# Performance work log

Measured on AMD Instinct MI355X. Metric: run time of the kernel, lower is better.

Reference implementation:

```python
import jax, jax.numpy as jnp
import numpy as np

OBS_DIM = 115
ID_LO, ID_HI = 97, 108  # one-hot agent-id slice


def setup_inputs() -> dict:
    key = jax.random.key(0)
    k1, k2 = jax.random.split(key)
    a, b, n_agents = 128, 512, 11
    state_dim = n_agents * OBS_DIM  # 1265
    agents_q = jax.random.normal(k1, (a, b, n_agents), dtype=jnp.float32)
    global_state = jax.random.normal(k2, (a, b, state_dim), dtype=jnp.float32)
    return {"agents_q": agents_q, "global_state": global_state}


def reference(agents_q, global_state):
    a, b, n_agents = agents_q.shape
    q = agents_q.reshape(-1, n_agents)                 # [B, A]
    gs = global_state.reshape(-1, global_state.shape[-1])  # [B, A*115]
    B = q.shape[0]

    ball_pos = gs[:, 88:90]                            # [B, 2]
    holder_info = gs[:, 94:97]
    is_my_team = holder_info[:, 1] != 0                # .bool() semantics
    goal = jnp.array([1.0, 0.0], dtype=q.dtype)
    ball_goal_dist = jnp.sqrt(jnp.sum((ball_pos - goal) ** 2, axis=1))
    valid_advance = is_my_team & (ball_goal_dist > 0.19) & (ball_goal_dist < 0.99)

    # all agent obs blocks at once: [B, A, 115]
    obs = gs[:, : n_agents * OBS_DIM].reshape(B, n_agents, OBS_DIM)
    agent_id = jnp.argmax(obs[:, :, ID_LO:ID_HI], axis=-1)        # [B, A] in [0,10]
    pos_x = jnp.take_along_axis(obs, (2 * agent_id)[..., None], axis=-1)[..., 0]
    pos_y = jnp.take_along_axis(obs, (2 * agent_id + 1)[..., None], axis=-1)[..., 0]

    # distance of each agent to ball and to goal: [B, A]
    dist_matrix = jnp.sqrt((pos_x - ball_pos[:, 0:1]) ** 2 + (pos_y - ball_pos[:, 1:2]) ** 2)
    goal_dist_matrix = jnp.sqrt((pos_x - 1.0) ** 2 + pos_y ** 2)

    holder_mask = jax.nn.one_hot(jnp.argmin(dist_matrix, axis=1), n_agents, dtype=q.dtype)
    advance_component = holder_mask * valid_advance[:, None].astype(q.dtype) * 5.0
    position_component = 1.0 / (goal_dist_matrix + 1e-6)
    combined = jnp.where(valid_advance[:, None], advance_component, position_component)

    weights = jax.nn.softmax(combined, axis=1)
    global_q = jnp.sum(q * weights, axis=1, keepdims=True)        # [B, 1]
    return (global_q * n_agents).reshape(a, b, 1)
```

## Files before the change

### kernel.cpp

```cpp
#include <hip/hip_runtime.h>
#include <math.h>

#define OBS_DIM 115
#define N_AGENTS 11

__global__ __launch_bounds__(256) void qmix_kernel(
    const float* __restrict__ q,
    const float* __restrict__ gs,
    float* __restrict__ out,
    int B)
{
    int r = blockIdx.x * blockDim.x + threadIdx.x;
    if (r >= B) return;

    const float* row = gs + (long)r * (N_AGENTS * OBS_DIM);

    float bx = row[88];
    float by = row[89];
    float team = row[95];
    float gx0 = bx - 1.0f;
    float ball_goal_dist = sqrtf(gx0 * gx0 + by * by);
    bool valid = (team != 0.0f) && (ball_goal_dist > 0.19f) && (ball_goal_dist < 0.99f);

    float dist[N_AGENTS];
    float gd[N_AGENTS];

    #pragma unroll
    for (int a = 0; a < N_AGENTS; ++a) {
        const float* base = row + a * OBS_DIM;
        float best = base[97];
        int bi = 0;
        #pragma unroll
        for (int j = 1; j < 11; ++j) {
            float v = base[97 + j];
            if (v > best) { best = v; bi = j; }
        }
        float px = base[2 * bi];
        float py = base[2 * bi + 1];
        float ddx = px - bx;
        float ddy = py - by;
        dist[a] = sqrtf(ddx * ddx + ddy * ddy);
        float ggx = px - 1.0f;
        gd[a] = sqrtf(ggx * ggx + py * py);
    }

    int holder = 0;
    float dmin = dist[0];
    #pragma unroll
    for (int a = 1; a < N_AGENTS; ++a) {
        if (dist[a] < dmin) { dmin = dist[a]; holder = a; }
    }

    float comb[N_AGENTS];
    float m = -INFINITY;
    #pragma unroll
    for (int a = 0; a < N_AGENTS; ++a) {
        float c;
        if (valid) {
            c = (a == holder) ? 5.0f : 0.0f;
        } else {
            c = 1.0f / (gd[a] + 1e-6f);
        }
        comb[a] = c;
        m = fmaxf(m, c);
    }

    const float* qr = q + (long)r * N_AGENTS;
    float s = 0.0f;
    float acc = 0.0f;
    #pragma unroll
    for (int a = 0; a < N_AGENTS; ++a) {
        float w = expf(comb[a] - m);
        s += w;
        acc += qr[a] * w;
    }

    out[r] = acc * (float)N_AGENTS / s;
}

extern "C" void kernel_launch(void* const* d_in, const int* in_sizes, int n_in,
                              void* d_out, int out_size, void* d_ws, size_t ws_size,
                              hipStream_t stream) {
    const float* q  = (const float*)d_in[0];
    const float* gs = (const float*)d_in[1];
    float* out = (float*)d_out;

    int B = in_sizes[0] / N_AGENTS;
    const int block = 256;
    int grid = (B + block - 1) / block;
    qmix_kernel<<<grid, block, 0, stream>>>(q, gs, out, B);
}
```

Measured before the change: 404.6 us.

## Stage needed row columns into shared memory via coalesced wave loads

Each block now handles 32 rows. Each wave cooperatively gathers only the columns needed (the position and one-hot slices, the ball and team fields, and q) into shared memory with lane-contiguous accesses, and then one thread per row computes the result from shared memory. This replaces per-thread strided, uncoalesced global loads. In exchange it uses about 49KB of LDS per block, which limits occupancy, and only 32 threads do the compute.

Result: slower. 419.0 us (+3.6%).

```diff
diff --git a/kernel.cpp b/kernel.cpp
--- a/kernel.cpp
+++ b/kernel.cpp
@@ -3,6 +3,9 @@
 
 #define OBS_DIM 115
 #define N_AGENTS 11
+#define ROWS 32
+#define SROW 385
+#define TELEM 377
 
 __global__ __launch_bounds__(256) void qmix_kernel(
     const float* __restrict__ q,
@@ -10,72 +13,112 @@
     float* __restrict__ out,
     int B)
 {
-    int r = blockIdx.x * blockDim.x + threadIdx.x;
-    if (r >= B) return;
+    __shared__ float sm[ROWS * SROW];
 
-    const float* row = gs + (long)r * (N_AGENTS * OBS_DIM);
+    const int tid  = threadIdx.x;
+    const int wave = tid >> 6;
+    const int lane = tid & 63;
+    const int row0 = blockIdx.x * ROWS;
 
-    float bx = row[88];
-    float by = row[89];
-    float team = row[95];
-    float gx0 = bx - 1.0f;
-    float ball_goal_dist = sqrtf(gx0 * gx0 + by * by);
-    bool valid = (team != 0.0f) && (ball_goal_dist > 0.19f) && (ball_goal_dist < 0.99f);
-
-    float dist[N_AGENTS];
-    float gd[N_AGENTS];
+    int cols[6];
+    #pragma unroll
+    for (int it = 0; it < 6; ++it) {
+        int o = it * 64 + lane;
+        int col;
+        if (o < 363) {
+            int a = o / 33;
+            int j = o - a * 33;
+            col = a * OBS_DIM + (j < 22 ? j : j + 75);
+        } else if (o == 363) col = 88;
+        else if (o == 364) col = 89;
+        else                col = 95;
+        cols[it] = col;
+    }
 
     #pragma unroll
-    for (int a = 0; a < N_AGENTS; ++a) {
-        const float* base = row + a * OBS_DIM;
-        float best = base[97];
-        int bi = 0;
+    for (int rr = 0; rr < 8; ++rr) {
+        int r = wave * 8 + rr;
+        int rg = row0 + r;
+        if (rg < B) {
+            long gbase = (long)rg * (N_AGENTS * OBS_DIM);
+            long qbase = (long)rg * N_AGENTS;
+            #pragma unroll
+            for (int it = 0; it < 6; ++it) {
+                int o = it * 64 + lane;
+                if (o < 366) {
+                    sm[r * SROW + o] = gs[gbase + cols[it]];
+                } else if (o < TELEM) {
+                    sm[r * SROW + o] = q[qbase + (o - 366)];
+                }
+            }
+        }
+    }
+    __syncthreads();
+
+    if (tid < ROWS && row0 + tid < B) {
+        const float* s = &sm[tid * SROW];
+
+        float bx = s[363];
+        float by = s[364];
+        float team = s[365];
+        float gx0 = bx - 1.0f;
+        float ball_goal_dist = sqrtf(gx0 * gx0 + by * by);
+        bool valid = (team != 0.0f) && (ball_goal_dist > 0.19f) && (ball_goal_dist < 0.99f);
+
+        float dist[N_AGENTS];
+        float gd[N_AGENTS];
+
         #pragma unroll
-        for (int j = 1; j < 11; ++j) {
-            float v = base[97 + j];
-            if (v > best) { best = v; bi = j; }
+        for (int a = 0; a < N_AGENTS; ++a) {
+            const float* base = s + a * 33;
+            float best = base[22];
+            int bi = 0;
+            #pragma unroll
+            for (int j = 1; j < 11; ++j) {
+                float v = base[22 + j];
+                if (v > best) { best = v; bi = j; }
+            }
+            float px = base[2 * bi];
+            float py = base[2 * bi + 1];
+            float ddx = px - bx;
+            float ddy = py - by;
+            dist[a] = sqrtf(ddx * ddx + ddy * ddy);
+            float ggx = px - 1.0f;
+            gd[a] = sqrtf(ggx * ggx + py * py);
         }
-        float px = base[2 * bi];
-        float py = base[2 * bi + 1];
-        float ddx = px - bx;
-        float ddy = py - by;
-        dist[a] = sqrtf(ddx * ddx + ddy * ddy);
-        float ggx = px - 1.0f;
-        gd[a] = sqrtf(ggx * ggx + py * py);
+
+        int holder = 0;
+        float dmin = dist[0];
+        #pragma unroll
+        for (int a = 1; a < N_AGENTS; ++a) {
+            if (dist[a] < dmin) { dmin = dist[a]; holder = a; }
+        }
+
+        float comb[N_AGENTS];
+        float m = -INFINITY;
+        #pragma unroll
+        for (int a = 0; a < N_AGENTS; ++a) {
+            float c;
+            if (valid) {
+                c = (a == holder) ? 5.0f : 0.0f;
+            } else {
+                c = 1.0f / (gd[a] + 1e-6f);
+            }
+            comb[a] = c;
+            m = fmaxf(m, c);
+        }
+
+        float ssum = 0.0f;
+        float acc = 0.0f;
+        #pragma unroll
+        for (int a = 0; a < N_AGENTS; ++a) {
+            float w = expf(comb[a] - m);
+            ssum += w;
+            acc += s[366 + a] * w;
+        }
+
+        out[row0 + tid] = acc * (float)N_AGENTS / ssum;
     }
-
-    int holder = 0;
-    float dmin = dist[0];
-    #pragma unroll
-    for (int a = 1; a < N_AGENTS; ++a) {
-        if (dist[a] < dmin) { dmin = dist[a]; holder = a; }
-    }
-
-    float comb[N_AGENTS];
-    float m = -INFINITY;
-    #pragma unroll
-    for (int a = 0; a < N_AGENTS; ++a) {
-        float c;
-        if (valid) {
-            c = (a == holder) ? 5.0f : 0.0f;
-        } else {
-            c = 1.0f / (gd[a] + 1e-6f);
-        }
-        comb[a] = c;
-        m = fmaxf(m, c);
-    }
-
-    const float* qr = q + (long)r * N_AGENTS;
-    float s = 0.0f;
-    float acc = 0.0f;
-    #pragma unroll
-    for (int a = 0; a < N_AGENTS; ++a) {
-        float w = expf(comb[a] - m);
-        s += w;
-        acc += qr[a] * w;
-    }
-
-    out[r] = acc * (float)N_AGENTS / s;
 }
 
 extern "C" void kernel_launch(void* const* d_in, const int* in_sizes, int n_in,
@@ -86,7 +129,6 @@
     float* out = (float*)d_out;
 
     int B = in_sizes[0] / N_AGENTS;
-    const int block = 256;
-    int grid = (B + block - 1) / block;
-    qmix_kernel<<<grid, block, 0, stream>>>(q, gs, out, B);
+    int grid = (B + ROWS - 1) / ROWS;
+    qmix_kernel<<<grid, 256, 0, stream>>>(q, gs, out, B);
 }
```

## Split each row across 16 threads, one per agent, with shuffle reductions

Applied to the files above, without the earlier changes.

Each batch row is now handled by a 16-lane group, with each active lane processing one agent's observation block. The argmin, max, and softmax sums are done with xor-shuffle reductions instead of serial loops in a single thread. The goal is more parallelism and better coalescing of the strided global_state reads, which were badly uncoalesced with one thread per row. In exchange, 5 of every 16 lanes sit idle, the ball/team loads are repeated by every lane in a group, and there are extra shuffle instructions.

After: 399.8 us. About the same (-1.2%).

```diff
diff --git a/kernel.cpp b/kernel.cpp
--- a/kernel.cpp
+++ b/kernel.cpp
@@ -3,6 +3,8 @@
 
 #define OBS_DIM 115
 #define N_AGENTS 11
+#define TPR 16
+#define ROWS_PER_BLOCK 16
 
 __global__ __launch_bounds__(256) void qmix_kernel(
     const float* __restrict__ q,
@@ -10,24 +12,28 @@
     float* __restrict__ out,
     int B)
 {
-    int r = blockIdx.x * blockDim.x + threadIdx.x;
+    const int tid = threadIdx.x;
+    const int g   = tid >> 4;
+    const int s   = tid & 15;
+    const int r   = blockIdx.x * ROWS_PER_BLOCK + g;
     if (r >= B) return;
 
-    const float* row = gs + (long)r * (N_AGENTS * OBS_DIM);
+    const float* row = gs + (size_t)r * (N_AGENTS * OBS_DIM);
 
     float bx = row[88];
     float by = row[89];
     float team = row[95];
-    float gx0 = bx - 1.0f;
-    float ball_goal_dist = sqrtf(gx0 * gx0 + by * by);
-    bool valid = (team != 0.0f) && (ball_goal_dist > 0.19f) && (ball_goal_dist < 0.99f);
+    float g0 = bx - 1.0f;
+    float bgd = sqrtf(g0 * g0 + by * by);
+    bool valid = (team != 0.0f) && (bgd > 0.19f) && (bgd < 0.99f);
 
-    float dist[N_AGENTS];
-    float gd[N_AGENTS];
+    float dist = INFINITY;
+    float comb = -INFINITY;
+    float qv = 0.0f;
+    float gd = 0.0f;
 
-    #pragma unroll
-    for (int a = 0; a < N_AGENTS; ++a) {
-        const float* base = row + a * OBS_DIM;
+    if (s < N_AGENTS) {
+        const float* base = row + s * OBS_DIM;
         float best = base[97];
         int bi = 0;
         #pragma unroll
@@ -37,45 +43,42 @@
         }
         float px = base[2 * bi];
         float py = base[2 * bi + 1];
-        float ddx = px - bx;
-        float ddy = py - by;
-        dist[a] = sqrtf(ddx * ddx + ddy * ddy);
-        float ggx = px - 1.0f;
-        gd[a] = sqrtf(ggx * ggx + py * py);
+        float dx = px - bx, dy = py - by;
+        dist = sqrtf(dx * dx + dy * dy);
+        float gx = px - 1.0f;
+        gd = sqrtf(gx * gx + py * py);
+        qv = q[(size_t)r * N_AGENTS + s];
     }
 
-    int holder = 0;
-    float dmin = dist[0];
+    int idx = s;
+    float d = dist;
     #pragma unroll
-    for (int a = 1; a < N_AGENTS; ++a) {
-        if (dist[a] < dmin) { dmin = dist[a]; holder = a; }
+    for (int off = 8; off >= 1; off >>= 1) {
+        float d2 = __shfl_xor(d, off, TPR);
+        int   i2 = __shfl_xor(idx, off, TPR);
+        if (d2 < d || (d2 == d && i2 < idx)) { d = d2; idx = i2; }
     }
 
-    float comb[N_AGENTS];
-    float m = -INFINITY;
-    #pragma unroll
-    for (int a = 0; a < N_AGENTS; ++a) {
-        float c;
-        if (valid) {
-            c = (a == holder) ? 5.0f : 0.0f;
-        } else {
-            c = 1.0f / (gd[a] + 1e-6f);
-        }
-        comb[a] = c;
-        m = fmaxf(m, c);
+    if (s < N_AGENTS) {
+        comb = valid ? ((s == idx) ? 5.0f : 0.0f)
+                     : 1.0f / (gd + 1e-6f);
     }
 
-    const float* qr = q + (long)r * N_AGENTS;
-    float s = 0.0f;
-    float acc = 0.0f;
+    float m = comb;
     #pragma unroll
-    for (int a = 0; a < N_AGENTS; ++a) {
-        float w = expf(comb[a] - m);
-        s += w;
-        acc += qr[a] * w;
+    for (int off = 8; off >= 1; off >>= 1)
+        m = fmaxf(m, __shfl_xor(m, off, TPR));
+
+    float w  = expf(comb - m);
+    float wq = w * qv;
+    #pragma unroll
+    for (int off = 8; off >= 1; off >>= 1) {
+        w  += __shfl_xor(w,  off, TPR);
+        wq += __shfl_xor(wq, off, TPR);
     }
 
-    out[r] = acc * (float)N_AGENTS / s;
+    if (s == 0)
+        out[r] = wq * (float)N_AGENTS / w;
 }
 
 extern "C" void kernel_launch(void* const* d_in, const int* in_sizes, int n_in,
@@ -86,7 +89,6 @@
     float* out = (float*)d_out;
 
     int B = in_sizes[0] / N_AGENTS;
-    const int block = 256;
-    int grid = (B + block - 1) / block;
-    qmix_kernel<<<grid, block, 0, stream>>>(q, gs, out, B);
+    int grid = (B + ROWS_PER_BLOCK - 1) / ROWS_PER_BLOCK;
+    qmix_kernel<<<grid, 256, 0, stream>>>(q, gs, out, B);
 }
```
